# Kernel tuning notes

Measured on AMD Instinct MI355X. Metric: run time of the kernel, lower is better.

The kernel has to match this reference:

```python
import jax, jax.numpy as jnp
import numpy as np

N, E, D_IN, H1, C1, D_OUT = 50000, 800000, 384, 4, 64, 5
D_HID = H1 * C1  # 256, input to layer 2


def setup_inputs() -> dict:
    key = jax.random.key(0)
    ks = jax.random.split(key, 12)

    def lin(k, i, o):
        return (jax.random.normal(k, (i, o), jnp.float32) / np.sqrt(i)).astype(jnp.float32)

    inp = {
        "x": jax.random.normal(ks[0], (N, D_IN), jnp.float32),
        "edge_index": jax.random.randint(ks[1], (2, E), 0, N, jnp.int32),
        # layer 1: TransformerConv(384 -> 64, heads=4, concat=True)
        "Wq1": lin(ks[2], D_IN, H1 * C1), "bq1": jnp.zeros((H1 * C1,), jnp.float32),
        "Wk1": lin(ks[3], D_IN, H1 * C1), "bk1": jnp.zeros((H1 * C1,), jnp.float32),
        "Wv1": lin(ks[4], D_IN, H1 * C1), "bv1": jnp.zeros((H1 * C1,), jnp.float32),
        "Ws1": lin(ks[5], D_IN, H1 * C1), "bs1": jnp.zeros((H1 * C1,), jnp.float32),
        # layer 2: TransformerConv(256 -> 5, heads=1, concat=False)
        "Wq2": lin(ks[6], D_HID, D_OUT), "bq2": jnp.zeros((D_OUT,), jnp.float32),
        "Wk2": lin(ks[7], D_HID, D_OUT), "bk2": jnp.zeros((D_OUT,), jnp.float32),
        "Wv2": lin(ks[8], D_HID, D_OUT), "bv2": jnp.zeros((D_OUT,), jnp.float32),
        "Ws2": lin(ks[9], D_HID, D_OUT), "bs2": jnp.zeros((D_OUT,), jnp.float32),
    }
    return inp


def _segment_softmax(logits, dst, n):
    # logits: [E, H] grouped by destination node
    m = jax.ops.segment_max(logits, dst, num_segments=n)
    m = jnp.where(jnp.isfinite(m), m, 0.0)
    e = jnp.exp(logits - m[dst])
    s = jax.ops.segment_sum(e, dst, num_segments=n)
    return e / (s[dst] + 1e-16)


def _transformer_conv(x, src, dst, Wq, bq, Wk, bk, Wv, bv, Ws, bs, heads, out_ch, concat):
    n = x.shape[0]
    q = (x @ Wq + bq).reshape(n, heads, out_ch)
    k = (x @ Wk + bk).reshape(n, heads, out_ch)
    v = (x @ Wv + bv).reshape(n, heads, out_ch)
    # per-edge attention logits: q_i . k_j / sqrt(C)   [E, H]
    logits = jnp.einsum('ehc,ehc->eh', q[dst], k[src]) / jnp.sqrt(jnp.float32(out_ch))
    alpha = _segment_softmax(logits, dst, n)          # [E, H]
    msg = v[src] * alpha[:, :, None]                  # [E, H, C]
    out = jax.ops.segment_sum(msg, dst, num_segments=n)  # [N, H, C]
    out = out.reshape(n, heads * out_ch) if concat else out.mean(axis=1)
    # root skip connection (root_weight=True default in PyG)
    return out + (x @ Ws + bs)


def reference(x, edge_index, Wq1, bq1, Wk1, bk1, Wv1, bv1, Ws1, bs1,
              Wq2, bq2, Wk2, bk2, Wv2, bv2, Ws2, bs2):
    src, dst = edge_index[0], edge_index[1]
    h = _transformer_conv(x, src, dst, Wq1, bq1, Wk1, bk1, Wv1, bv1, Ws1, bs1,
                          H1, C1, True)
    h = jax.nn.relu(h)
    out = _transformer_conv(h, src, dst, Wq2, bq2, Wk2, bk2, Wv2, bv2, Ws2, bs2,
                            1, D_OUT, False)
    return out
```

## Files before the change

### kernel.cpp

```cpp
#include <hip/hip_runtime.h>
#include <hip/hip_bf16.h>

#define N_NODES 50000
#define N_EDGES 800000
#define NPAD    50048
#define SCAN_B  196
#define HIST_B  3125
#define PW1_B   1536
#define PW2_B   32
#define GEMM_B  (((NPAD / 128 + 7) / 8) * 32)
#define SCAT_B  ((N_EDGES + 511) / 512)

typedef __attribute__((ext_vector_type(8))) short bf16x8;
typedef __attribute__((ext_vector_type(8))) unsigned short u16x8;
typedef __attribute__((ext_vector_type(4))) float f32x4;

__device__ __forceinline__ unsigned short f2bf(float f) {
  union { float f; unsigned u; } x; x.f = f;
  unsigned r = x.u + 0x7fffu + ((x.u >> 16) & 1u);
  return (unsigned short)(r >> 16);
}
__device__ __forceinline__ float bf2f(unsigned short u) {
  union { unsigned u; float f; } x; x.u = ((unsigned)u) << 16;
  return x.f;
}
__device__ __forceinline__ unsigned pkbf(float lo, float hi) {
  return ((unsigned)f2bf(hi) << 16) | f2bf(lo);
}
__device__ __forceinline__ unsigned char enc8v(float v) {
  float t = fminf(fmaxf(fmaf(v, 16.f, 128.5f), 0.f), 255.f);
  return (unsigned char)(int)t;
}
__device__ __forceinline__ char enc8k(float v) {
  float t = fminf(fmaxf(v * 16.f, -127.f), 127.f);
  return (char)(int)floorf(t + 0.5f);
}
__device__ __forceinline__ char enc8q(float v) {
  float t = fminf(fmaxf(v * 24.f, -127.f), 127.f);
  return (char)(int)floorf(t + 0.5f);
}

__device__ __forceinline__ int dot4i8(int a, int b, int c) {
#if __has_builtin(__builtin_amdgcn_sdot4)
  return __builtin_amdgcn_sdot4(a, b, c, false);
#else
  int r = c;
  r += (int)(char)(a) * (int)(char)(b);
  r += (int)(char)(a >> 8) * (int)(char)(b >> 8);
  r += (int)(char)(a >> 16) * (int)(char)(b >> 16);
  r += (int)(char)(a >> 24) * (int)(char)(b >> 24);
  return r;
#endif
}

__device__ __forceinline__ void gload16(const void* g, void* l) {
  __builtin_amdgcn_global_load_lds(
      (const __attribute__((address_space(1))) unsigned int*)g,
      (__attribute__((address_space(3))) unsigned int*)l, 16, 0, 0);
}

__global__ __launch_bounds__(256) void scan1_kernel(const int* __restrict__ counts,
                                                    int* __restrict__ tmp, int* __restrict__ bsum, int n) {
  __shared__ int sm[256];
  int i = blockIdx.x * 256 + threadIdx.x;
  int v = (i < n) ? counts[i] : 0;
  sm[threadIdx.x] = v;
  __syncthreads();
  for (int off = 1; off < 256; off <<= 1) {
    int t = (threadIdx.x >= off) ? sm[threadIdx.x - off] : 0;
    __syncthreads();
    sm[threadIdx.x] += t;
    __syncthreads();
  }
  if (i < n) tmp[i] = sm[threadIdx.x] - v;
  if (threadIdx.x == 255) bsum[blockIdx.x] = sm[255];
}

__global__ __launch_bounds__(256) void scan2_kernel(const int* __restrict__ bsum,
                                                    int* __restrict__ bbase, int nb) {
  __shared__ int sm[256];
  int v = (threadIdx.x < nb) ? bsum[threadIdx.x] : 0;
  sm[threadIdx.x] = v;
  __syncthreads();
  for (int off = 1; off < 256; off <<= 1) {
    int t = (threadIdx.x >= off) ? sm[threadIdx.x - off] : 0;
    __syncthreads();
    sm[threadIdx.x] += t;
    __syncthreads();
  }
  if (threadIdx.x < nb) bbase[threadIdx.x] = sm[threadIdx.x] - v;
}

__global__ __launch_bounds__(256) void scan3_kernel(const int* __restrict__ tmp,
                                                    const int* __restrict__ bbase,
                                                    int* __restrict__ offsets, int* __restrict__ cursor,
                                                    int n, int E) {
  int i = blockIdx.x * 256 + threadIdx.x;
  if (i < n) {
    int o = tmp[i] + bbase[blockIdx.x];
    offsets[i] = o;
    cursor[i] = o;
  }
  if (i == 0) offsets[n] = E;
}

__global__ __launch_bounds__(256) void prep_kernel(
    const int* __restrict__ edst, int* __restrict__ counts,
    const float* __restrict__ Wq1, const float* __restrict__ Wk1,
    const float* __restrict__ Wv1, const float* __restrict__ Ws1,
    const float* __restrict__ bq1, const float* __restrict__ bk1,
    const float* __restrict__ bv1, const float* __restrict__ bs1,
    unsigned short* __restrict__ wbt, float* __restrict__ bias1,
    const float* __restrict__ Wq2, const float* __restrict__ Wk2,
    const float* __restrict__ Wv2, const float* __restrict__ Ws2,
    const float* __restrict__ bq2, const float* __restrict__ bk2,
    const float* __restrict__ bv2, const float* __restrict__ bs2,
    unsigned short* __restrict__ w2bt, float* __restrict__ bias2) {
  int b = blockIdx.x;
  if (b < HIST_B) {
    int e = b * 256 + threadIdx.x;
    if (e < N_EDGES) atomicAdd(&counts[edst[e]], 1);
  } else if (b < HIST_B + PW1_B) {
    int idx = (b - HIST_B) * 256 + threadIdx.x;
    int n = idx / 384, k = idx - n * 384;
    int blk = n >> 8, cc = n & 255;
    const float* W = (blk == 0) ? Wq1 : (blk == 1) ? Wk1 : (blk == 2) ? Wv1 : Ws1;
    wbt[idx] = f2bf(W[(long)k * 256 + cc]);
    if (k == 0) {
      const float* bb = (blk == 0) ? bq1 : (blk == 1) ? bk1 : (blk == 2) ? bv1 : bs1;
      bias1[n] = bb[cc];
    }
  } else {
    int idx = (b - HIST_B - PW1_B) * 256 + threadIdx.x;
    int c = idx >> 8, p = idx & 255;
    unsigned short o = 0;
    if (c < 20) {
      int blk = c / 5, cc = c - blk * 5;
      int tch = (p & 0xC0) + (p & 3) * 16 + ((p & 63) >> 2);
      const float* W = (blk == 0) ? Wq2 : (blk == 1) ? Wk2 : (blk == 2) ? Wv2 : Ws2;
      o = f2bf(W[(long)tch * 5 + cc]);
      if (p == 0) {
        const float* bb = (blk == 0) ? bq2 : (blk == 1) ? bk2 : (blk == 2) ? bv2 : bs2;
        bias2[c] = bb[cc];
      }
    }
    w2bt[idx] = o;
  }
}

__global__ __launch_bounds__(512) void gemm_scatter_kernel(
    const float* __restrict__ x, const unsigned short* __restrict__ wbt,
    const float* __restrict__ bias,
    char* __restrict__ qb8, unsigned char* __restrict__ kvb,
    unsigned short* __restrict__ s1b,
    const int* __restrict__ esrc, const int* __restrict__ edst,
    int* __restrict__ cursor, int* __restrict__ csr_src) {
  __shared__ unsigned short As[128 * 64];
  __shared__ unsigned short Bs[256 * 64];
  int bid = blockIdx.x;
  if (bid >= GEMM_B) {
    int e = (bid - GEMM_B) * 512 + threadIdx.x;
    if (e < N_EDGES) {
      int pos = atomicAdd(&cursor[edst[e]], 1);
      csr_src[pos] = esrc[e];
    }
    return;
  }
  int grp = bid >> 5, bl = bid & 31;
  int mx = grp * 8 + (bl & 7);
  int y = bl >> 3;
  if (mx >= NPAD / 128) return;
  int tid = threadIdx.x;
  long m0 = (long)mx * 128;
  int n0 = y * 256;
  int w = tid >> 6, l = tid & 63;
  int wr = (w >> 2) * 64, wc = (w & 3) * 64;
  int lr = l & 15, c0 = l >> 4;
  int lj = lr & 7;
  f32x4 acc[4][4] = {};
  int ra = tid >> 3, cs = tid & 7;
  int cg = cs ^ (ra & 7);
  long ar0 = m0 + ra;      if (ar0 > (long)(N_NODES - 1)) ar0 = N_NODES - 1;
  long ar1 = m0 + 64 + ra; if (ar1 > (long)(N_NODES - 1)) ar1 = N_NODES - 1;
  const float* gA0 = x + ar0 * 384 + cg * 8;
  const float* gA1 = x + ar1 * 384 + cg * 8;
  unsigned short* aw0 = &As[ra * 64 + cs * 8];
  unsigned short* aw1 = &As[(ra + 64) * 64 + cs * 8];
  const unsigned short* gB[4];
#pragma unroll
  for (int r = 0; r < 4; ++r)
    gB[r] = wbt + (long)(n0 + ra + r * 64) * 384 + cg * 8;
  float4 a00 = *(const float4*)gA0, a01 = *(const float4*)(gA0 + 4);
  float4 a10 = *(const float4*)gA1, a11 = *(const float4*)(gA1 + 4);
  for (int kt = 0; kt < 6; ++kt) {
    int ko = kt * 64;
    __syncthreads();
#pragma unroll
    for (int r = 0; r < 4; ++r)
      gload16(gB[r] + ko, &Bs[(tid + r * 512) * 8]);
    {
      union { bf16x8 v; unsigned u[4]; } t;
      t.u[0] = pkbf(a00.x, a00.y); t.u[1] = pkbf(a00.z, a00.w);
      t.u[2] = pkbf(a01.x, a01.y); t.u[3] = pkbf(a01.z, a01.w);
      *(bf16x8*)aw0 = t.v;
      t.u[0] = pkbf(a10.x, a10.y); t.u[1] = pkbf(a10.z, a10.w);
      t.u[2] = pkbf(a11.x, a11.y); t.u[3] = pkbf(a11.z, a11.w);
      *(bf16x8*)aw1 = t.v;
    }
    __syncthreads();
    if (kt < 5) {
      a00 = *(const float4*)(gA0 + ko + 64); a01 = *(const float4*)(gA0 + ko + 68);
      a10 = *(const float4*)(gA1 + ko + 64); a11 = *(const float4*)(gA1 + ko + 68);
    }
#pragma unroll
    for (int ks = 0; ks < 2; ++ks) {
      int pc = ((ks * 4 + c0) ^ lj) * 8;
      bf16x8 af[4], bfv[4];
#pragma unroll
      for (int mf = 0; mf < 4; ++mf)
        af[mf] = *(const bf16x8*)&As[(wr + mf * 16 + lr) * 64 + pc];
#pragma unroll
      for (int nf = 0; nf < 4; ++nf)
        bfv[nf] = *(const bf16x8*)&Bs[(wc + nf * 16 + lr) * 64 + pc];
#pragma unroll
      for (int mf = 0; mf < 4; ++mf)
#pragma unroll
        for (int nf = 0; nf < 4; ++nf)
          acc[mf][nf] = __builtin_amdgcn_mfma_f32_16x16x32_bf16(af[mf], bfv[nf], acc[mf][nf], 0, 0, 0);
    }
  }
  float bv[4];
#pragma unroll
  for (int nf = 0; nf < 4; ++nf) bv[nf] = bias[n0 + wc + nf * 16 + lr];
  int pos = wc + lr * 4;
#pragma unroll
  for (int mf = 0; mf < 4; ++mf) {
#pragma unroll
    for (int i = 0; i < 4; ++i) {
      long row = m0 + wr + mf * 16 + c0 * 4 + i;
      float v0 = acc[mf][0][i] + bv[0];
      float v1 = acc[mf][1][i] + bv[1];
      float v2 = acc[mf][2][i] + bv[2];
      float v3 = acc[mf][3][i] + bv[3];
      if (y == 0) {
        char4 st; st.x = enc8q(v0); st.y = enc8q(v1); st.z = enc8q(v2); st.w = enc8q(v3);
        *(char4*)&qb8[row * 256 + pos] = st;
      } else if (y == 1) {
        char4 st; st.x = enc8k(v0); st.y = enc8k(v1); st.z = enc8k(v2); st.w = enc8k(v3);
        *(char4*)&kvb[row * 512 + pos] = st;
      } else if (y == 2) {
        uchar4 st; st.x = enc8v(v0); st.y = enc8v(v1); st.z = enc8v(v2); st.w = enc8v(v3);
        *(uchar4*)&kvb[row * 512 + 256 + pos] = st;
      } else {
        ushort4 st; st.x = f2bf(v0); st.y = f2bf(v1); st.z = f2bf(v2); st.w = f2bf(v3);
        *(ushort4*)&s1b[row * 256 + pos] = st;
      }
    }
  }
}

__global__ __launch_bounds__(256) void agg1_kernel(
    const char* __restrict__ qb8, const unsigned char* __restrict__ kvb,
    unsigned short* s1b,
    const int* __restrict__ offsets, const int* __restrict__ csr_src) {
  int w = threadIdx.x >> 6, l = threadIdx.x & 63;
  int g = l >> 4;
  int sub = l & 15;
  for (int n = blockIdx.x * 4 + w; n < N_NODES; n += gridDim.x * 4) {
    int i0 = offsets[n], i1 = offsets[n + 1];
    long ob = (long)n * 256 + sub * 16;
    if (i0 >= i1) {
      if (g == 0) {
        u16x8 sv0 = *(const u16x8*)&s1b[ob];
        u16x8 sv1 = *(const u16x8*)&s1b[ob + 8];
        u16x8 h0, h1;
#pragma unroll
        for (int j = 0; j < 8; ++j) {
          h0[j] = (short)f2bf(fmaxf(bf2f((unsigned short)sv0[j]), 0.f));
          h1[j] = (short)f2bf(fmaxf(bf2f((unsigned short)sv1[j]), 0.f));
        }
        *(u16x8*)&s1b[ob] = h0;
        *(u16x8*)&s1b[ob + 8] = h1;
      }
      continue;
    }
    int4 qi = *(const int4*)&qb8[(long)n * 256 + sub * 16];
    float acc[16] = {};
    float se = 0.f;

    auto ldbatch = [&](int i, int4& ka, uint4& va, int4& kw, uint4& vw) {
      int ia = i + g, ib = i + 4 + g;
      int sa = csr_src[ia < i1 ? ia : i1 - 1];
      int sb = csr_src[ib < i1 ? ib : i1 - 1];
      const char* ba = (const char*)kvb + (long)sa * 512 + sub * 16;
      const char* bb = (const char*)kvb + (long)sb * 512 + sub * 16;
      ka = *(const int4*)ba; va = *(const uint4*)(ba + 256);
      kw = *(const int4*)bb; vw = *(const uint4*)(bb + 256);
    };
#define VACC(E, W, B) \
    acc[(B) + 0] = fmaf(E, (float)((W) & 0xffu), acc[(B) + 0]); \
    acc[(B) + 1] = fmaf(E, (float)(((W) >> 8) & 0xffu), acc[(B) + 1]); \
    acc[(B) + 2] = fmaf(E, (float)(((W) >> 16) & 0xffu), acc[(B) + 2]); \
    acc[(B) + 3] = fmaf(E, (float)((W) >> 24), acc[(B) + 3]);
    auto consume = [&](int i, int4 ka, uint4 va, int4 kw, uint4 vw) {
      int ia = i + g, ib = i + 4 + g;
      int da = 0, db = 0;
      da = dot4i8(qi.x, ka.x, da); da = dot4i8(qi.y, ka.y, da);
      da = dot4i8(qi.z, ka.z, da); da = dot4i8(qi.w, ka.w, da);
      db = dot4i8(qi.x, kw.x, db); db = dot4i8(qi.y, kw.y, db);
      db = dot4i8(qi.z, kw.z, db); db = dot4i8(qi.w, kw.w, db);
      da += __shfl_xor(da, 1); da += __shfl_xor(da, 2);
      db += __shfl_xor(db, 1); db += __shfl_xor(db, 2);
      float ea = (ia < i1) ? __expf((float)da * (1.f / 3072.f)) : 0.f;
      float eb = (ib < i1) ? __expf((float)db * (1.f / 3072.f)) : 0.f;
      se += ea + eb;
      VACC(ea, va.x, 0) VACC(ea, va.y, 4) VACC(ea, va.z, 8) VACC(ea, va.w, 12)
      VACC(eb, vw.x, 0) VACC(eb, vw.y, 4) VACC(eb, vw.z, 8) VACC(eb, vw.w, 12)
    };

    int i = i0;
    int4 ka0, kw0; uint4 va0, vw0;
    ldbatch(i, ka0, va0, kw0, vw0);
    for (; i + 8 < i1; i += 8) {
      int4 ka1, kw1; uint4 va1, vw1;
      ldbatch(i + 8, ka1, va1, kw1, vw1);
      consume(i, ka0, va0, kw0, vw0);
      ka0 = ka1; va0 = va1; kw0 = kw1; vw0 = vw1;
    }
    consume(i, ka0, va0, kw0, vw0);
#undef VACC
#pragma unroll
    for (int j = 0; j < 16; ++j) {
      acc[j] += __shfl_xor(acc[j], 16);
      acc[j] += __shfl_xor(acc[j], 32);
    }
    se += __shfl_xor(se, 16);
    se += __shfl_xor(se, 32);
    if (g == 0) {
      float inv = (se > 0.f) ? 1.0f / se : 0.f;
      float bias = (se > 0.f) ? -8.0f : 0.f;
      u16x8 sv0 = *(const u16x8*)&s1b[ob];
      u16x8 sv1 = *(const u16x8*)&s1b[ob + 8];
      u16x8 h0, h1;
#pragma unroll
      for (int j = 0; j < 8; ++j) {
        float v0 = fmaf(acc[j] * inv, 0.0625f, bias);
        float v1 = fmaf(acc[8 + j] * inv, 0.0625f, bias);
        h0[j] = (short)f2bf(fmaxf(v0 + bf2f((unsigned short)sv0[j]), 0.f));
        h1[j] = (short)f2bf(fmaxf(v1 + bf2f((unsigned short)sv1[j]), 0.f));
      }
      *(u16x8*)&s1b[ob] = h0;
      *(u16x8*)&s1b[ob + 8] = h1;
    }
  }
}

__global__ __launch_bounds__(256) void lin2_kernel(const unsigned short* __restrict__ hb,
                                                   const unsigned short* __restrict__ w2bt,
                                                   const float* __restrict__ bias2,
                                                   float* __restrict__ qs2, float* __restrict__ kv2) {
  __shared__ unsigned short Bs2[32 * 264];
  __shared__ float bsh[32];
  for (int i = threadIdx.x; i < 32 * 32; i += 256) {
    int r = i >> 5, cc = i & 31;
    *(u16x8*)&Bs2[r * 264 + cc * 8] = *(const u16x8*)&w2bt[r * 256 + cc * 8];
  }
  if (threadIdx.x < 32) bsh[threadIdx.x] = (threadIdx.x < 20) ? bias2[threadIdx.x] : 0.f;
  __syncthreads();
  int w = threadIdx.x >> 6, l = threadIdx.x & 63;
  long row0 = (long)blockIdx.x * 128 + w * 32;
  int lr = l & 15, c0 = l >> 4;
  f32x4 acc[2][2] = {};
  for (int kk = 0; kk < 8; ++kk) {
    int koff = kk * 32 + c0 * 8;
    bf16x8 af[2], bfv[2];
    af[0] = *(const bf16x8*)&hb[(row0 + lr) * 256 + koff];
    af[1] = *(const bf16x8*)&hb[(row0 + 16 + lr) * 256 + koff];
    bfv[0] = *(const bf16x8*)&Bs2[lr * 264 + koff];
    bfv[1] = *(const bf16x8*)&Bs2[(16 + lr) * 264 + koff];
#pragma unroll
    for (int mf = 0; mf < 2; ++mf)
#pragma unroll
      for (int nf = 0; nf < 2; ++nf)
        acc[mf][nf] = __builtin_amdgcn_mfma_f32_16x16x32_bf16(af[mf], bfv[nf], acc[mf][nf], 0, 0, 0);
  }
#pragma unroll
  for (int mf = 0; mf < 2; ++mf) {
#pragma unroll
    for (int nf = 0; nf < 2; ++nf) {
      int col = nf * 16 + lr;
#pragma unroll
      for (int i = 0; i < 4; ++i) {
        long n = row0 + mf * 16 + c0 * 4 + i;
        float v = acc[mf][nf][i] + bsh[col];
        if (col < 5) qs2[n * 12 + col] = v;
        else if (col < 15) kv2[n * 12 + (col - 5)] = v;
        else if (col < 20) qs2[n * 12 + (col - 10)] = v;
      }
    }
  }
}

__global__ void agg2_kernel(const float* __restrict__ qs2, const float* __restrict__ kv2,
                            const int* __restrict__ offsets, const int* __restrict__ csr_src,
                            float* __restrict__ out) {
  int n = blockIdx.x * 256 + threadIdx.x;
  if (n >= N_NODES) return;
  const float* bn = &qs2[(long)n * 12];
  const float is5 = 0.4472135954999579f;
  float q[5], acc[5] = {0, 0, 0, 0, 0}, se = 0.f;
#pragma unroll
  for (int c = 0; c < 5; ++c) q[c] = bn[c] * is5;
  int i0 = offsets[n], i1 = offsets[n + 1];
  for (int i = i0; i < i1; ++i) {
    int s = csr_src[i];
    const float4* ps = (const float4*)&kv2[(long)s * 12];
    float4 A = ps[0], B = ps[1], C = ps[2];
    float lg = q[0] * A.x + q[1] * A.y + q[2] * A.z + q[3] * A.w + q[4] * B.x;
    float ee = __expf(lg);
    se += ee;
    acc[0] += ee * B.y; acc[1] += ee * B.z; acc[2] += ee * B.w;
    acc[3] += ee * C.x; acc[4] += ee * C.y;
  }
  float inv = 1.f / (se + 1e-16f);
#pragma unroll
  for (int c = 0; c < 5; ++c) out[(long)n * 5 + c] = acc[c] * inv + bn[5 + c];
}

extern "C" void kernel_launch(void* const* d_in, const int* in_sizes, int n_in,
                              void* d_out, int out_size, void* d_ws, size_t ws_size,
                              hipStream_t stream) {
  (void)in_sizes; (void)n_in; (void)out_size; (void)ws_size;
  const float* x   = (const float*)d_in[0];
  const int* eidx  = (const int*)d_in[1];
  const int* esrc  = eidx;
  const int* edst  = eidx + N_EDGES;
  const float* Wq1 = (const float*)d_in[2];  const float* bq1 = (const float*)d_in[3];
  const float* Wk1 = (const float*)d_in[4];  const float* bk1 = (const float*)d_in[5];
  const float* Wv1 = (const float*)d_in[6];  const float* bv1 = (const float*)d_in[7];
  const float* Ws1 = (const float*)d_in[8];  const float* bs1 = (const float*)d_in[9];
  const float* Wq2 = (const float*)d_in[10]; const float* bq2 = (const float*)d_in[11];
  const float* Wk2 = (const float*)d_in[12]; const float* bk2 = (const float*)d_in[13];
  const float* Wv2 = (const float*)d_in[14]; const float* bv2 = (const float*)d_in[15];
  const float* Ws2 = (const float*)d_in[16]; const float* bs2 = (const float*)d_in[17];

  char* p = (char*)d_ws;
  auto take = [&](size_t bytes) { char* r = p; p += (bytes + 255) & ~(size_t)255; return r; };
  unsigned short* wbt = (unsigned short*)take((size_t)1024 * 384 * 2);
  float* bias1        = (float*)take(1024 * 4);
  char* qb8           = (char*)take((size_t)NPAD * 256);
  unsigned char* kvb  = (unsigned char*)take((size_t)NPAD * 512);
  unsigned short* s1b = (unsigned short*)take((size_t)NPAD * 256 * 2);
  unsigned short* w2bt = (unsigned short*)take(32 * 256 * 2);
  float* bias2        = (float*)take(32 * 4);
  float* qs2          = (float*)take((size_t)NPAD * 12 * 4);
  float* kv2          = (float*)take((size_t)NPAD * 12 * 4);
  int* counts         = (int*)take((size_t)N_NODES * 4);
  int* offsets        = (int*)take((size_t)(N_NODES + 1) * 4);
  int* cursor         = (int*)take((size_t)N_NODES * 4);
  int* csr_src        = (int*)take((size_t)N_EDGES * 4);
  int* scan_tmp       = (int*)take((size_t)N_NODES * 4);
  int* scan_bsum      = (int*)take(256 * 4);
  int* scan_bbase     = (int*)take(256 * 4);

  hipMemsetAsync(counts, 0, (size_t)N_NODES * 4, stream);
  prep_kernel<<<HIST_B + PW1_B + PW2_B, 256, 0, stream>>>(
      edst, counts, Wq1, Wk1, Wv1, Ws1, bq1, bk1, bv1, bs1, wbt, bias1,
      Wq2, Wk2, Wv2, Ws2, bq2, bk2, bv2, bs2, w2bt, bias2);
  scan1_kernel<<<SCAN_B, 256, 0, stream>>>(counts, scan_tmp, scan_bsum, N_NODES);
  scan2_kernel<<<1, 256, 0, stream>>>(scan_bsum, scan_bbase, SCAN_B);
  scan3_kernel<<<SCAN_B, 256, 0, stream>>>(scan_tmp, scan_bbase, offsets, cursor, N_NODES, N_EDGES);
  gemm_scatter_kernel<<<GEMM_B + SCAT_B, 512, 0, stream>>>(
      x, wbt, bias1, qb8, kvb, s1b, esrc, edst, cursor, csr_src);
  agg1_kernel<<<2048, 256, 0, stream>>>(qb8, kvb, s1b, offsets, csr_src);
  lin2_kernel<<<NPAD / 128, 256, 0, stream>>>(s1b, w2bt, bias2, qs2, kv2);
  agg2_kernel<<<(N_NODES + 255) / 256, 256, 0, stream>>>(qs2, kv2, offsets, csr_src, (float*)d_out);
}
```

Measured before the change: 236.0 us.

## Fuse three scan kernels into one grid-synced scan; double-buffer GEMM B tiles

Replaces the three-kernel exclusive scan with one kernel in which each block publishes its sum, spins on a global counter until every block is done, then reduces the preceding block sums to get its base. This removes two launches and the temporary buffers. The GEMM now double-buffers the weight tile in LDS, issuing the async load for the next k-step before computing the current one so the global-to-LDS copy overlaps the MFMA work. The spin barrier relies on all 196 blocks being resident at once, and doubling Bs raises LDS use per block, which may lower GEMM occupancy.

```diff
diff --git a/kernel.cpp b/kernel.cpp
--- a/kernel.cpp
+++ b/kernel.cpp
@@ -59,8 +59,12 @@
       (__attribute__((address_space(3))) unsigned int*)l, 16, 0, 0);
 }
 
-__global__ __launch_bounds__(256) void scan1_kernel(const int* __restrict__ counts,
-                                                    int* __restrict__ tmp, int* __restrict__ bsum, int n) {
+__global__ __launch_bounds__(256) void scan_kernel(const int* __restrict__ counts,
+                                                   int* __restrict__ offsets,
+                                                   int* __restrict__ cursor,
+                                                   int* __restrict__ bsum,
+                                                   int* __restrict__ done,
+                                                   int n, int E) {
   __shared__ int sm[256];
   int i = blockIdx.x * 256 + threadIdx.x;
   int v = (i < n) ? counts[i] : 0;
@@ -72,32 +76,28 @@
     sm[threadIdx.x] += t;
     __syncthreads();
   }
-  if (i < n) tmp[i] = sm[threadIdx.x] - v;
-  if (threadIdx.x == 255) bsum[blockIdx.x] = sm[255];
-}
-
-__global__ __launch_bounds__(256) void scan2_kernel(const int* __restrict__ bsum,
-                                                    int* __restrict__ bbase, int nb) {
-  __shared__ int sm[256];
-  int v = (threadIdx.x < nb) ? bsum[threadIdx.x] : 0;
-  sm[threadIdx.x] = v;
+  int local_ex = sm[threadIdx.x] - v;
+  if (threadIdx.x == 255) {
+    bsum[blockIdx.x] = sm[255];
+    __threadfence();
+    atomicAdd(done, 1);
+  }
+  if (threadIdx.x == 0) {
+    while (atomicAdd(done, 0) < (int)gridDim.x) { }
+  }
   __syncthreads();
-  for (int off = 1; off < 256; off <<= 1) {
-    int t = (threadIdx.x >= off) ? sm[threadIdx.x - off] : 0;
+  int base = 0;
+  for (int jj = threadIdx.x; jj < (int)blockIdx.x; jj += 256)
+    base += atomicAdd(&bsum[jj], 0);
+  sm[threadIdx.x] = base;
+  __syncthreads();
+  for (int off = 128; off > 0; off >>= 1) {
+    if (threadIdx.x < off) sm[threadIdx.x] += sm[threadIdx.x + off];
     __syncthreads();
-    sm[threadIdx.x] += t;
-    __syncthreads();
-  }
-  if (threadIdx.x < nb) bbase[threadIdx.x] = sm[threadIdx.x] - v;
-}
-
-__global__ __launch_bounds__(256) void scan3_kernel(const int* __restrict__ tmp,
-                                                    const int* __restrict__ bbase,
-                                                    int* __restrict__ offsets, int* __restrict__ cursor,
-                                                    int n, int E) {
-  int i = blockIdx.x * 256 + threadIdx.x;
+  }
+  base = sm[0];
   if (i < n) {
-    int o = tmp[i] + bbase[blockIdx.x];
+    int o = base + local_ex;
     offsets[i] = o;
     cursor[i] = o;
   }
@@ -156,7 +156,7 @@
     const int* __restrict__ esrc, const int* __restrict__ edst,
     int* __restrict__ cursor, int* __restrict__ csr_src) {
   __shared__ unsigned short As[128 * 64];
-  __shared__ unsigned short Bs[256 * 64];
+  __shared__ unsigned short Bs[2 * 256 * 64];
   int bid = blockIdx.x;
   if (bid >= GEMM_B) {
     int e = (bid - GEMM_B) * 512 + threadIdx.x;
@@ -192,12 +192,12 @@
     gB[r] = wbt + (long)(n0 + ra + r * 64) * 384 + cg * 8;
   float4 a00 = *(const float4*)gA0, a01 = *(const float4*)(gA0 + 4);
   float4 a10 = *(const float4*)gA1, a11 = *(const float4*)(gA1 + 4);
+#pragma unroll
+  for (int r = 0; r < 4; ++r)
+    gload16(gB[r], &Bs[(tid + r * 512) * 8]);
   for (int kt = 0; kt < 6; ++kt) {
-    int ko = kt * 64;
+    int b = kt & 1;
     __syncthreads();
-#pragma unroll
-    for (int r = 0; r < 4; ++r)
-      gload16(gB[r] + ko, &Bs[(tid + r * 512) * 8]);
     {
       union { bf16x8 v; unsigned u[4]; } t;
       t.u[0] = pkbf(a00.x, a00.y); t.u[1] = pkbf(a00.z, a00.w);
@@ -209,9 +209,14 @@
     }
     __syncthreads();
     if (kt < 5) {
-      a00 = *(const float4*)(gA0 + ko + 64); a01 = *(const float4*)(gA0 + ko + 68);
-      a10 = *(const float4*)(gA1 + ko + 64); a11 = *(const float4*)(gA1 + ko + 68);
-    }
+      int ko2 = (kt + 1) * 64;
+#pragma unroll
+      for (int r = 0; r < 4; ++r)
+        gload16(gB[r] + ko2, &Bs[(b ^ 1) * 16384 + (tid + r * 512) * 8]);
+      a00 = *(const float4*)(gA0 + ko2); a01 = *(const float4*)(gA0 + ko2 + 4);
+      a10 = *(const float4*)(gA1 + ko2); a11 = *(const float4*)(gA1 + ko2 + 4);
+    }
+    const unsigned short* Bb = &Bs[b * 16384];
 #pragma unroll
     for (int ks = 0; ks < 2; ++ks) {
       int pc = ((ks * 4 + c0) ^ lj) * 8;
@@ -221,7 +226,7 @@
         af[mf] = *(const bf16x8*)&As[(wr + mf * 16 + lr) * 64 + pc];
 #pragma unroll
       for (int nf = 0; nf < 4; ++nf)
-        bfv[nf] = *(const bf16x8*)&Bs[(wc + nf * 16 + lr) * 64 + pc];
+        bfv[nf] = *(const bf16x8*)&Bb[(wc + nf * 16 + lr) * 64 + pc];
 #pragma unroll
       for (int mf = 0; mf < 4; ++mf)
 #pragma unroll
@@ -455,21 +460,19 @@
   float* bias2        = (float*)take(32 * 4);
   float* qs2          = (float*)take((size_t)NPAD * 12 * 4);
   float* kv2          = (float*)take((size_t)NPAD * 12 * 4);
-  int* counts         = (int*)take((size_t)N_NODES * 4);
+  int* counts         = (int*)take((size_t)(N_NODES + 64) * 4);
+  int* scan_done      = counts + N_NODES;
   int* offsets        = (int*)take((size_t)(N_NODES + 1) * 4);
   int* cursor         = (int*)take((size_t)N_NODES * 4);
   int* csr_src        = (int*)take((size_t)N_EDGES * 4);
-  int* scan_tmp       = (int*)take((size_t)N_NODES * 4);
   int* scan_bsum      = (int*)take(256 * 4);
-  int* scan_bbase     = (int*)take(256 * 4);
-
-  hipMemsetAsync(counts, 0, (size_t)N_NODES * 4, stream);
+
+  hipMemsetAsync(counts, 0, (size_t)(N_NODES + 64) * 4, stream);
   prep_kernel<<<HIST_B + PW1_B + PW2_B, 256, 0, stream>>>(
       edst, counts, Wq1, Wk1, Wv1, Ws1, bq1, bk1, bv1, bs1, wbt, bias1,
       Wq2, Wk2, Wv2, Ws2, bq2, bk2, bv2, bs2, w2bt, bias2);
-  scan1_kernel<<<SCAN_B, 256, 0, stream>>>(counts, scan_tmp, scan_bsum, N_NODES);
-  scan2_kernel<<<1, 256, 0, stream>>>(scan_bsum, scan_bbase, SCAN_B);
-  scan3_kernel<<<SCAN_B, 256, 0, stream>>>(scan_tmp, scan_bbase, offsets, cursor, N_NODES, N_EDGES);
+  scan_kernel<<<SCAN_B, 256, 0, stream>>>(counts, offsets, cursor, scan_bsum,
+                                          scan_done, N_NODES, N_EDGES);
   gemm_scatter_kernel<<<GEMM_B + SCAT_B, 512, 0, stream>>>(
       x, wbt, bias1, qb8, kvb, s1b, esrc, edst, cursor, csr_src);
   agg1_kernel<<<2048, 256, 0, stream>>>(qb8, kvb, s1b, offsets, csr_src);
```

After: 259.7 us. 10.0% more time.

## Fuse layer-1 aggregation with layer-2 linear projection in one kernel

Applied to the files above, without the earlier changes.

Merges agg1 and lin2 into one kernel. Each wave keeps its node's ReLU'd hidden vector in registers and computes the 20 layer-2 projection outputs with a per-lane dot product against bf16 weights staged in shared memory, reduced by shuffles. This drops the bf16 write-back of the hidden state and the separate GEMM kernel's re-read and launch. In exchange it uses 16KB of LDS per block, adds scalar FMA work and shuffle reductions per node in place of MFMA, and rounds the hidden state differently because it stays fp32 instead of going through bf16.

```diff
diff --git a/kernel.cpp b/kernel.cpp
--- a/kernel.cpp
+++ b/kernel.cpp
@@ -259,144 +259,108 @@
   }
 }
 
-__global__ __launch_bounds__(256) void agg1_kernel(
+__global__ __launch_bounds__(256) void agg1lin2_kernel(
     const char* __restrict__ qb8, const unsigned char* __restrict__ kvb,
-    unsigned short* s1b,
-    const int* __restrict__ offsets, const int* __restrict__ csr_src) {
+    const unsigned short* __restrict__ s1b,
+    const unsigned short* __restrict__ w2bt, const float* __restrict__ bias2,
+    const int* __restrict__ offsets, const int* __restrict__ csr_src,
+    float* __restrict__ qs2, float* __restrict__ kv2) {
+  __shared__ unsigned short w2s[32 * 256];
+  __shared__ float bsh[32];
+  for (int i = threadIdx.x; i < 1024; i += 256)
+    *(u16x8*)&w2s[i * 8] = *(const u16x8*)&w2bt[i * 8];
+  if (threadIdx.x < 32) bsh[threadIdx.x] = (threadIdx.x < 20) ? bias2[threadIdx.x] : 0.f;
+  __syncthreads();
   int w = threadIdx.x >> 6, l = threadIdx.x & 63;
   int g = l >> 4;
   int sub = l & 15;
   for (int n = blockIdx.x * 4 + w; n < N_NODES; n += gridDim.x * 4) {
     int i0 = offsets[n], i1 = offsets[n + 1];
-    long ob = (long)n * 256 + sub * 16;
-    if (i0 >= i1) {
-      if (g == 0) {
-        u16x8 sv0 = *(const u16x8*)&s1b[ob];
-        u16x8 sv1 = *(const u16x8*)&s1b[ob + 8];
-        u16x8 h0, h1;
-#pragma unroll
-        for (int j = 0; j < 8; ++j) {
-          h0[j] = (short)f2bf(fmaxf(bf2f((unsigned short)sv0[j]), 0.f));
-          h1[j] = (short)f2bf(fmaxf(bf2f((unsigned short)sv1[j]), 0.f));
-        }
-        *(u16x8*)&s1b[ob] = h0;
-        *(u16x8*)&s1b[ob + 8] = h1;
-      }
-      continue;
-    }
-    int4 qi = *(const int4*)&qb8[(long)n * 256 + sub * 16];
     float acc[16] = {};
     float se = 0.f;
-
-    auto ldbatch = [&](int i, int4& ka, uint4& va, int4& kw, uint4& vw) {
-      int ia = i + g, ib = i + 4 + g;
-      int sa = csr_src[ia < i1 ? ia : i1 - 1];
-      int sb = csr_src[ib < i1 ? ib : i1 - 1];
-      const char* ba = (const char*)kvb + (long)sa * 512 + sub * 16;
-      const char* bb = (const char*)kvb + (long)sb * 512 + sub * 16;
-      ka = *(const int4*)ba; va = *(const uint4*)(ba + 256);
-      kw = *(const int4*)bb; vw = *(const uint4*)(bb + 256);
-    };
+    if (i0 < i1) {
+      int4 qi = *(const int4*)&qb8[(long)n * 256 + sub * 16];
+      auto ldbatch = [&](int i, int4& ka, uint4& va, int4& kw, uint4& vw) {
+        int ia = i + g, ib = i + 4 + g;
+        int sa = csr_src[ia < i1 ? ia : i1 - 1];
+        int sb = csr_src[ib < i1 ? ib : i1 - 1];
+        const char* ba = (const char*)kvb + (long)sa * 512 + sub * 16;
+        const char* bb = (const char*)kvb + (long)sb * 512 + sub * 16;
+        ka = *(const int4*)ba; va = *(const uint4*)(ba + 256);
+        kw = *(const int4*)bb; vw = *(const uint4*)(bb + 256);
+      };
 #define VACC(E, W, B) \
-    acc[(B) + 0] = fmaf(E, (float)((W) & 0xffu), acc[(B) + 0]); \
-    acc[(B) + 1] = fmaf(E, (float)(((W) >> 8) & 0xffu), acc[(B) + 1]); \
-    acc[(B) + 2] = fmaf(E, (float)(((W) >> 16) & 0xffu), acc[(B) + 2]); \
-    acc[(B) + 3] = fmaf(E, (float)((W) >> 24), acc[(B) + 3]);
-    auto consume = [&](int i, int4 ka, uint4 va, int4 kw, uint4 vw) {
-      int ia = i + g, ib = i + 4 + g;
-      int da = 0, db = 0;
-      da = dot4i8(qi.x, ka.x, da); da = dot4i8(qi.y, ka.y, da);
-      da = dot4i8(qi.z, ka.z, da); da = dot4i8(qi.w, ka.w, da);
-      db = dot4i8(qi.x, kw.x, db); db = dot4i8(qi.y, kw.y, db);
-      db = dot4i8(qi.z, kw.z, db); db = dot4i8(qi.w, kw.w, db);
-      da += __shfl_xor(da, 1); da += __shfl_xor(da, 2);
-      db += __shfl_xor(db, 1); db += __shfl_xor(db, 2);
-      float ea = (ia < i1) ? __expf((float)da * (1.f / 3072.f)) : 0.f;
-      float eb = (ib < i1) ? __expf((float)db * (1.f / 3072.f)) : 0.f;
-      se += ea + eb;
-      VACC(ea, va.x, 0) VACC(ea, va.y, 4) VACC(ea, va.z, 8) VACC(ea, va.w, 12)
-      VACC(eb, vw.x, 0) VACC(eb, vw.y, 4) VACC(eb, vw.z, 8) VACC(eb, vw.w, 12)
-    };
-
-    int i = i0;
-    int4 ka0, kw0; uint4 va0, vw0;
-    ldbatch(i, ka0, va0, kw0, vw0);
-    for (; i + 8 < i1; i += 8) {
-      int4 ka1, kw1; uint4 va1, vw1;
-      ldbatch(i + 8, ka1, va1, kw1, vw1);
+      acc[(B) + 0] = fmaf(E, (float)((W) & 0xffu), acc[(B) + 0]); \
+      acc[(B) + 1] = fmaf(E, (float)(((W) >> 8) & 0xffu), acc[(B) + 1]); \
+      acc[(B) + 2] = fmaf(E, (float)(((W) >> 16) & 0xffu), acc[(B) + 2]); \
+      acc[(B) + 3] = fmaf(E, (float)((W) >> 24), acc[(B) + 3]);
+      auto consume = [&](int i, int4 ka, uint4 va, int4 kw, uint4 vw) {
+        int ia = i + g, ib = i + 4 + g;
+        int da = 0, db = 0;
+        da = dot4i8(qi.x, ka.x, da); da = dot4i8(qi.y, ka.y, da);
+        da = dot4i8(qi.z, ka.z, da); da = dot4i8(qi.w, ka.w, da);
+        db = dot4i8(qi.x, kw.x, db); db = dot4i8(qi.y, kw.y, db);
+        db = dot4i8(qi.z, kw.z, db); db = dot4i8(qi.w, kw.w, db);
+        da += __shfl_xor(da, 1); da += __shfl_xor(da, 2);
+        db += __shfl_xor(db, 1); db += __shfl_xor(db, 2);
+        float ea = (ia < i1) ? __expf((float)da * (1.f / 3072.f)) : 0.f;
+        float eb = (ib < i1) ? __expf((float)db * (1.f / 3072.f)) : 0.f;
+        se += ea + eb;
+        VACC(ea, va.x, 0) VACC(ea, va.y, 4) VACC(ea, va.z, 8) VACC(ea, va.w, 12)
+        VACC(eb, vw.x, 0) VACC(eb, vw.y, 4) VACC(eb, vw.z, 8) VACC(eb, vw.w, 12)
+      };
+      int i = i0;
+      int4 ka0, kw0; uint4 va0, vw0;
+      ldbatch(i, ka0, va0, kw0, vw0);
+      for (; i + 8 < i1; i += 8) {
+        int4 ka1, kw1; uint4 va1, vw1;
+        ldbatch(i + 8, ka1, va1, kw1, vw1);
+        consume(i, ka0, va0, kw0, vw0);
+        ka0 = ka1; va0 = va1; kw0 = kw1; vw0 = vw1;
+      }
       consume(i, ka0, va0, kw0, vw0);
-      ka0 = ka1; va0 = va1; kw0 = kw1; vw0 = vw1;
-    }
-    consume(i, ka0, va0, kw0, vw0);
 #undef VACC
 #pragma unroll
-    for (int j = 0; j < 16; ++j) {
-      acc[j] += __shfl_xor(acc[j], 16);
-      acc[j] += __shfl_xor(acc[j], 32);
-    }
-    se += __shfl_xor(se, 16);
-    se += __shfl_xor(se, 32);
-    if (g == 0) {
-      float inv = (se > 0.f) ? 1.0f / se : 0.f;
-      float bias = (se > 0.f) ? -8.0f : 0.f;
-      u16x8 sv0 = *(const u16x8*)&s1b[ob];
-      u16x8 sv1 = *(const u16x8*)&s1b[ob + 8];
-      u16x8 h0, h1;
-#pragma unroll
-      for (int j = 0; j < 8; ++j) {
-        float v0 = fmaf(acc[j] * inv, 0.0625f, bias);
-        float v1 = fmaf(acc[8 + j] * inv, 0.0625f, bias);
-        h0[j] = (short)f2bf(fmaxf(v0 + bf2f((unsigned short)sv0[j]), 0.f));
-        h1[j] = (short)f2bf(fmaxf(v1 + bf2f((unsigned short)sv1[j]), 0.f));
+      for (int j = 0; j < 16; ++j) {
+        acc[j] += __shfl_xor(acc[j], 16);
+        acc[j] += __shfl_xor(acc[j], 32);
       }
-      *(u16x8*)&s1b[ob] = h0;
-      *(u16x8*)&s1b[ob + 8] = h1;
-    }
-  }
-}
-
-__global__ __launch_bounds__(256) void lin2_kernel(const unsigned short* __restrict__ hb,
-                                                   const unsigned short* __restrict__ w2bt,
-                                                   const float* __restrict__ bias2,
-                                                   float* __restrict__ qs2, float* __restrict__ kv2) {
-  __shared__ unsigned short Bs2[32 * 264];
-  __shared__ float bsh[32];
-  for (int i = threadIdx.x; i < 32 * 32; i += 256) {
-    int r = i >> 5, cc = i & 31;
-    *(u16x8*)&Bs2[r * 264 + cc * 8] = *(const u16x8*)&w2bt[r * 256 + cc * 8];
-  }
-  if (threadIdx.x < 32) bsh[threadIdx.x] = (threadIdx.x < 20) ? bias2[threadIdx.x] : 0.f;
-  __syncthreads();
-  int w = threadIdx.x >> 6, l = threadIdx.x & 63;
-  long row0 = (long)blockIdx.x * 128 + w * 32;
-  int lr = l & 15, c0 = l >> 4;
-  f32x4 acc[2][2] = {};
-  for (int kk = 0; kk < 8; ++kk) {
-    int koff = kk * 32 + c0 * 8;
-    bf16x8 af[2], bfv[2];
-    af[0] = *(const bf16x8*)&hb[(row0 + lr) * 256 + koff];
-    af[1] = *(const bf16x8*)&hb[(row0 + 16 + lr) * 256 + koff];
-    bfv[0] = *(const bf16x8*)&Bs2[lr * 264 + koff];
-    bfv[1] = *(const bf16x8*)&Bs2[(16 + lr) * 264 + koff];
-#pragma unroll
-    for (int mf = 0; mf < 2; ++mf)
-#pragma unroll
-      for (int nf = 0; nf < 2; ++nf)
-        acc[mf][nf] = __builtin_amdgcn_mfma_f32_16x16x32_bf16(af[mf], bfv[nf], acc[mf][nf], 0, 0, 0);
-  }
-#pragma unroll
-  for (int mf = 0; mf < 2; ++mf) {
-#pragma unroll
-    for (int nf = 0; nf < 2; ++nf) {
-      int col = nf * 16 + lr;
-#pragma unroll
-      for (int i = 0; i < 4; ++i) {
-        long n = row0 + mf * 16 + c0 * 4 + i;
-        float v = acc[mf][nf][i] + bsh[col];
-        if (col < 5) qs2[n * 12 + col] = v;
-        else if (col < 15) kv2[n * 12 + (col - 5)] = v;
-        else if (col < 20) qs2[n * 12 + (col - 10)] = v;
-      }
+      se += __shfl_xor(se, 16);
+      se += __shfl_xor(se, 32);
+    }
+    float inv = (se > 0.f) ? 1.0f / se : 0.f;
+    float vb_ = (se > 0.f) ? -8.0f : 0.f;
+    long ob = (long)n * 256 + sub * 16;
+    u16x8 sv0 = *(const u16x8*)&s1b[ob];
+    u16x8 sv1 = *(const u16x8*)&s1b[ob + 8];
+    float h[16];
+#pragma unroll
+    for (int j = 0; j < 8; ++j) {
+      h[j]     = fmaxf(fmaf(acc[j] * inv, 0.0625f, vb_) + bf2f((unsigned short)sv0[j]), 0.f);
+      h[8 + j] = fmaxf(fmaf(acc[8 + j] * inv, 0.0625f, vb_) + bf2f((unsigned short)sv1[j]), 0.f);
+    }
+    float s5[5];
+#pragma unroll
+    for (int c = 0; c < 5; ++c) {
+      const unsigned short* wrow = &w2s[(g * 5 + c) * 256 + sub * 16];
+      u16x8 w0 = *(const u16x8*)wrow;
+      u16x8 w1 = *(const u16x8*)(wrow + 8);
+      float s = 0.f;
+#pragma unroll
+      for (int j = 0; j < 8; ++j)
+        s += h[j] * bf2f((unsigned short)w0[j]) + h[8 + j] * bf2f((unsigned short)w1[j]);
+      s += __shfl_xor(s, 1); s += __shfl_xor(s, 2);
+      s += __shfl_xor(s, 4); s += __shfl_xor(s, 8);
+      s5[c] = s;
+    }
+    if (sub < 5) {
+      float v = (sub == 0 ? s5[0] : sub == 1 ? s5[1] : sub == 2 ? s5[2]
+                 : sub == 3 ? s5[3] : s5[4]) + bsh[g * 5 + sub];
+      long nb = (long)n * 12;
+      if (g == 0)      qs2[nb + sub] = v;
+      else if (g == 1) kv2[nb + sub] = v;
+      else if (g == 2) kv2[nb + 5 + sub] = v;
+      else             qs2[nb + 5 + sub] = v;
     }
   }
 }
@@ -472,7 +436,7 @@
   scan3_kernel<<<SCAN_B, 256, 0, stream>>>(scan_tmp, scan_bbase, offsets, cursor, N_NODES, N_EDGES);
   gemm_scatter_kernel<<<GEMM_B + SCAT_B, 512, 0, stream>>>(
       x, wbt, bias1, qb8, kvb, s1b, esrc, edst, cursor, csr_src);
-  agg1_kernel<<<2048, 256, 0, stream>>>(qb8, kvb, s1b, offsets, csr_src);
-  lin2_kernel<<<NPAD / 128, 256, 0, stream>>>(s1b, w2bt, bias2, qs2, kv2);
+  agg1lin2_kernel<<<2048, 256, 0, stream>>>(qb8, kvb, s1b, w2bt, bias2,
+                                            offsets, csr_src, qs2, kv2);
   agg2_kernel<<<(N_NODES + 255) / 256, 256, 0, stream>>>(qs2, kv2, offsets, csr_src, (float*)d_out);
 }
```

After: 249.4 us. 5.7% more time.
